# Kernel tuning notes

Hardware: AMD Instinct MI355X
Metric: run time of the kernel (lower is better)

The kernel has to match this reference:

```python
import jax, jax.numpy as jnp
import numpy as np

B, S, D, H, DFF = 4, 2048, 768, 12, 3072
DK = D // H

def setup_inputs() -> dict:
    key = jax.random.key(0)
    ks = jax.random.split(key, 16)
    sc = 0.02
    inp = {
        'src': jax.random.normal(ks[0], (B, S, D), jnp.float32),
        'mask': jnp.ones((B, 1, 1, S), jnp.int32),
        'Wq': jax.random.normal(ks[1], (D, D), jnp.float32) * sc,
        'bq': jnp.zeros((D,), jnp.float32),
        'Wk': jax.random.normal(ks[2], (D, D), jnp.float32) * sc,
        'bk': jnp.zeros((D,), jnp.float32),
        'Wv': jax.random.normal(ks[3], (D, D), jnp.float32) * sc,
        'bv': jnp.zeros((D,), jnp.float32),
        'Wo': jax.random.normal(ks[4], (D, D), jnp.float32) * sc,
        'bo': jnp.zeros((D,), jnp.float32),
        'W1': jax.random.normal(ks[5], (D, DFF), jnp.float32) * sc,
        'b1': jnp.zeros((DFF,), jnp.float32),
        'W2': jax.random.normal(ks[6], (DFF, D), jnp.float32) * sc,
        'b2': jnp.zeros((D,), jnp.float32),
        'ln1_g': jnp.ones((D,), jnp.float32), 'ln1_b': jnp.zeros((D,), jnp.float32),
        'ln2_g': jnp.ones((D,), jnp.float32), 'ln2_b': jnp.zeros((D,), jnp.float32),
    }
    return inp

def _layernorm(x, g, b, eps=1e-5):
    mu = jnp.mean(x, axis=-1, keepdims=True)
    var = jnp.mean(jnp.square(x - mu), axis=-1, keepdims=True)
    return (x - mu) * jax.lax.rsqrt(var + eps) * g + b

def reference(src, mask, Wq, bq, Wk, bk, Wv, bv, Wo, bo, W1, b1, W2, b2, ln1_g, ln1_b, ln2_g, ln2_b):
    # Multi-head self-attention (dropout in eval mode -> identity)
    q = (src @ Wq + bq).reshape(B, S, H, DK).transpose(0, 2, 1, 3)  # [B,H,S,dk]
    k = (src @ Wk + bk).reshape(B, S, H, DK).transpose(0, 2, 1, 3)
    v = (src @ Wv + bv).reshape(B, S, H, DK).transpose(0, 2, 1, 3)
    scores = jnp.einsum('bhqd,bhkd->bhqk', q, k) / jnp.sqrt(jnp.float32(DK))
    scores = jnp.where(mask == 0, jnp.float32(-1e9), scores)
    attn = jax.nn.softmax(scores, axis=-1)
    ctx = jnp.einsum('bhqk,bhkd->bhqd', attn, v)  # [B,H,S,dk]
    ctx = ctx.transpose(0, 2, 1, 3).reshape(B, S, D)
    attn_out = ctx @ Wo + bo
    x = _layernorm(src + attn_out, ln1_g, ln1_b)
    ffn = jax.nn.relu(x @ W1 + b1) @ W2 + b2
    return _layernorm(x + ffn, ln2_g, ln2_b)
```

## Files before the change

kernel.cpp:

```cpp
#include <hip/hip_runtime.h>
#include <hip/hip_bf16.h>
#include <stdint.h>

constexpr int BB = 4;
constexpr int SS = 2048;
constexpr int DD = 768;
constexpr int HH = 12;
constexpr int DKK = 64;
constexpr int DFF2 = 3072;
constexpr int MR = BB * SS;

typedef __attribute__((ext_vector_type(4))) short short4v;
typedef __attribute__((ext_vector_type(8))) short short8v;
typedef __attribute__((ext_vector_type(4))) float f32x4;
typedef __attribute__((ext_vector_type(16))) float f32x16;
typedef __attribute__((ext_vector_type(4))) float float4v;
typedef __attribute__((ext_vector_type(4))) unsigned int u32x4;

static __device__ inline short f2bs(float f) {
    __hip_bfloat16 h = __float2bfloat16(f);
    return (short)__builtin_bit_cast(unsigned short, h);
}
static __device__ inline float bs2f(short s) {
    __hip_bfloat16 h = __builtin_bit_cast(__hip_bfloat16, (unsigned short)s);
    return __bfloat162float(h);
}

static __device__ inline void glds16(const void* g, void* l) {
    __builtin_amdgcn_global_load_lds(
        (const __attribute__((address_space(1))) void*)g,
        (__attribute__((address_space(3))) void*)l, 16, 0, 0);
}

static __device__ inline unsigned cvtpk(float a, float b) {
    unsigned d;
    asm("v_cvt_pk_bf16_f32 %0, %1, %2" : "=v"(d) : "v"(a), "v"(b));
    return d;
}
static __device__ inline short8v pk4(unsigned a, unsigned b, unsigned c, unsigned d) {
    u32x4 w; w[0] = a; w[1] = b; w[2] = c; w[3] = d;
    return __builtin_bit_cast(short8v, w);
}

static __device__ inline void bar_vmcnt4() {
    __builtin_amdgcn_sched_barrier(0);
    asm volatile("s_waitcnt vmcnt(4)" ::: "memory");
    __builtin_amdgcn_s_barrier();
    __builtin_amdgcn_sched_barrier(0);
}
static __device__ inline void bar_vmcnt0() {
    __builtin_amdgcn_sched_barrier(0);
    asm volatile("s_waitcnt vmcnt(0)" ::: "memory");
    __builtin_amdgcn_s_barrier();
    __builtin_amdgcn_sched_barrier(0);
}
static __device__ inline void bar_plain() {
    __builtin_amdgcn_sched_barrier(0);
    __builtin_amdgcn_s_barrier();
    __builtin_amdgcn_sched_barrier(0);
}

__global__ __launch_bounds__(256) void cast_f32_bf16(const float* __restrict__ in,
                                                     short* __restrict__ out, int n) {
    int i = (blockIdx.x * 256 + threadIdx.x) * 4;
    if (i < n) {
        float4v v = *(const float4v*)&in[i];
        short4v o;
        o[0] = f2bs(v[0]); o[1] = f2bs(v[1]); o[2] = f2bs(v[2]); o[3] = f2bs(v[3]);
        *(short4v*)&out[i] = o;
    }
}

__global__ __launch_bounds__(256) void transpose_cast(const float* __restrict__ W,
                                                      short* __restrict__ Wt, int K, int N) {
    __shared__ float tile[32][33];
    int n0 = blockIdx.x * 32, k0 = blockIdx.y * 32;
    int tx = threadIdx.x & 31, ty = threadIdx.x >> 5;
    #pragma unroll
    for (int i = 0; i < 32; i += 8)
        tile[ty + i][tx] = W[(size_t)(k0 + ty + i) * N + n0 + tx];
    __syncthreads();
    #pragma unroll
    for (int i = 0; i < 32; i += 8)
        Wt[(size_t)(n0 + ty + i) * K + k0 + tx] = f2bs(tile[tx][ty + i]);
}

__global__ __launch_bounds__(256) void vtrans(const short* __restrict__ V,
                                              short* __restrict__ Vt) {
    __shared__ short t[64][72];
    const int tid = threadIdx.x;
    const size_t base = (size_t)blockIdx.y * SS * DKK;
    const int s0 = blockIdx.x * 64;
    int r = tid >> 3, c = (tid & 7) * 8;
    #pragma unroll
    for (int it = 0; it < 2; it++)
        *(short8v*)&t[it * 32 + r][c] =
            *(const short8v*)&V[base + (size_t)(s0 + it * 32 + r) * DKK + c];
    __syncthreads();
    int d = tid >> 2, grp = (tid & 3) * 16;
    short8v o0, o1;
    #pragma unroll
    for (int e = 0; e < 8; e++) {
        int p0 = e, p1 = 8 + e;
        o0[e] = t[grp + (p0 & 3) + 8 * ((p0 >> 2) & 1) + 4 * (p0 >> 3)][d];
        o1[e] = t[grp + (p1 & 3) + 8 * ((p1 >> 2) & 1) + 4 * (p1 >> 3)][d];
    }
    int c0 = 2 * (tid & 3), c1 = c0 + 1;
    int p0 = c0 ^ (d & 7), p1 = c1 ^ (d & 7);
    *(short8v*)&Vt[base + (size_t)d * SS + s0 + p0 * 8] = o0;
    *(short8v*)&Vt[base + (size_t)d * SS + s0 + p1 * 8] = o1;
}

template <int EPI>
__global__ __launch_bounds__(256) void gemm_bt(
    const short* __restrict__ A, const short* __restrict__ Bt,
    int Nn, int Kn,
    const float* __restrict__ bias0, const float* __restrict__ bias1,
    const float* __restrict__ bias2,
    short* __restrict__ out0, short* __restrict__ out1, short* __restrict__ out2) {
    __shared__ alignas(16) short sA[3][128 * 32];
    __shared__ alignas(16) short sB[3][128 * 32];
    const int tid = threadIdx.x;
    const int wave = tid >> 6, lane = tid & 63;
    const int g = lane >> 4, qq = lane & 15;
    const int wm = (wave >> 1) * 64, wn = (wave & 1) * 64;

    const int gx = gridDim.x;
    const int nwg = gx * gridDim.y;
    const int wgid = blockIdx.y * gx + blockIdx.x;
    const int cpx = nwg >> 3;
    const int swz = (wgid & 7) * cpx + (wgid >> 3);
    const int bx = swz % gx, by = swz / gx;
    const int m0 = by * 128, n0 = bx * 128;

    const int e0 = wave * 512 + lane * 8;
    const int r0 = e0 >> 5, c0 = e0 & 31;

    const f32x4 zero = {0.0f, 0.0f, 0.0f, 0.0f};
    f32x4 acc[4][4];
    #pragma unroll
    for (int i = 0; i < 4; i++)
        #pragma unroll
        for (int j = 0; j < 4; j++) acc[i][j] = zero;

    const int NK = Kn >> 5;
    glds16(&A[(size_t)(m0 + r0) * Kn + c0], &sA[0][wave * 512]);
    glds16(&A[(size_t)(m0 + r0 + 64) * Kn + c0], &sA[0][wave * 512 + 2048]);
    glds16(&Bt[(size_t)(n0 + r0) * Kn + c0], &sB[0][wave * 512]);
    glds16(&Bt[(size_t)(n0 + r0 + 64) * Kn + c0], &sB[0][wave * 512 + 2048]);
    __syncthreads();

    int cur = 0, nxt = 1;
    for (int kt = 0; kt < NK; ++kt) {
        if (kt + 1 < NK) {
            const int k1 = (kt + 1) * 32;
            glds16(&A[(size_t)(m0 + r0) * Kn + k1 + c0], &sA[nxt][wave * 512]);
            glds16(&A[(size_t)(m0 + r0 + 64) * Kn + k1 + c0], &sA[nxt][wave * 512 + 2048]);
            glds16(&Bt[(size_t)(n0 + r0) * Kn + k1 + c0], &sB[nxt][wave * 512]);
            glds16(&Bt[(size_t)(n0 + r0 + 64) * Kn + k1 + c0], &sB[nxt][wave * 512 + 2048]);
            bar_vmcnt4();
        } else {
            bar_vmcnt0();
        }
        short8v af[4], bf[4];
        #pragma unroll
        for (int i = 0; i < 4; i++) {
            af[i] = *(const short8v*)&sA[cur][(wm + i * 16 + qq) * 32 + 8 * g];
            bf[i] = *(const short8v*)&sB[cur][(wn + i * 16 + qq) * 32 + 8 * g];
        }
        #pragma unroll
        for (int i = 0; i < 4; i++)
            #pragma unroll
            for (int j = 0; j < 4; j++)
                acc[i][j] = __builtin_amdgcn_mfma_f32_16x16x32_bf16(af[i], bf[j], acc[i][j], 0, 0, 0);
        cur = nxt;
        nxt = (nxt == 2) ? 0 : nxt + 1;
    }

    if constexpr (EPI == 2) {
        int which = bx / 6;
        const float* bias = (which == 0) ? bias0 : ((which == 1) ? bias1 : bias2);
        short* outp = (which == 0) ? out0 : ((which == 1) ? out1 : out2);
        float scale = (which == 0) ? 0.125f * 1.44269504088896f : 1.0f;
        #pragma unroll
        for (int i = 0; i < 4; i++)
            #pragma unroll
            for (int j = 0; j < 4; j++)
                #pragma unroll
                for (int r = 0; r < 4; r++) {
                    int row = m0 + wm + i * 16 + g * 4 + r;
                    int col = n0 - which * DD + wn + j * 16 + qq;
                    float vv = (acc[i][j][r] + bias[col]) * scale;
                    int b_ = row >> 11, s_ = row & 2047;
                    int h_ = col >> 6, d_ = col & 63;
                    if (which == 1)
                        d_ = (((d_ >> 3) ^ (s_ & 7)) << 3) | (d_ & 7);
                    outp[(((size_t)(b_ * HH + h_)) * SS + s_) * DKK + d_] = f2bs(vv);
                }
    } else {
        #pragma unroll
        for (int i = 0; i < 4; i++)
            #pragma unroll
            for (int j = 0; j < 4; j++)
                #pragma unroll
                for (int r = 0; r < 4; r++) {
                    int row = m0 + wm + i * 16 + g * 4 + r;
                    int col = n0 + wn + j * 16 + qq;
                    float vv = acc[i][j][r] + bias0[col];
                    if (EPI == 1) vv = fmaxf(vv, 0.0f);
                    out0[(size_t)row * Nn + col] = f2bs(vv);
                }
    }
}

__global__ __launch_bounds__(256) void attn_kernel(
    const short* __restrict__ Q, const short* __restrict__ Kb,
    const short* __restrict__ Vt, const int* __restrict__ mask,
    short* __restrict__ ctx) {
    __shared__ alignas(16) short sK[2][64 * 64];
    __shared__ alignas(16) short sV[2][64 * 64];
    __shared__ float sAl[4][32];
    __shared__ unsigned char smask[256];
    const int tid = threadIdx.x;
    const int wave = tid >> 6, lane = tid & 63;
    const int hi = lane >> 5, ln = lane & 31;
    constexpr int NT = SS / 64;

    int flat = blockIdx.y * gridDim.x + blockIdx.x;
    int nw = (flat & 7) * 96 + (flat >> 3);
    const int bh = nw >> 4, qb = nw & 15;
    const int b_ = bh / HH, h_ = bh % HH;
    const int q0 = qb * 128 + wave * 32;
    const size_t base = (size_t)bh * SS * DKK;

    {
        const int* mp = mask + b_ * SS + tid * 8;
        unsigned char by = 0;
        #pragma unroll
        for (int e = 0; e < 8; e++) by |= (unsigned char)((mp[e] != 0) << e);
        smask[tid] = by;
    }

    short8v qf[4];
    {
        const short* qp = &Q[base + (size_t)(q0 + ln) * DKK];
        #pragma unroll
        for (int c = 0; c < 4; c++)
            qf[c] = *(const short8v*)(qp + 16 * c + 8 * hi);
    }

    f32x16 O0, O1, ZEROV;
    #pragma unroll
    for (int r = 0; r < 16; r++) { O0[r] = 0.0f; O1[r] = 0.0f; ZEROV[r] = 0.0f; }
    float lreg = 0.0f;

    const int stgrow = wave * 8 + (lane >> 3);
    const int stgc = (lane & 7) * 8;
    const int rsz = (ln & 7) << 4;

    glds16(&Kb[base + (size_t)stgrow * DKK + stgc], &sK[0][wave * 512]);
    glds16(&Kb[base + (size_t)(stgrow + 32) * DKK + stgc], &sK[0][2048 + wave * 512]);
    glds16(&Vt[base + (size_t)stgrow * SS + stgc], &sV[0][wave * 512]);
    glds16(&Vt[base + (size_t)(stgrow + 32) * SS + stgc], &sV[0][2048 + wave * 512]);
    glds16(&Kb[base + (size_t)(64 + stgrow) * DKK + stgc], &sK[1][wave * 512]);
    glds16(&Kb[base + (size_t)(64 + stgrow + 32) * DKK + stgc], &sK[1][2048 + wave * 512]);
    glds16(&Vt[base + (size_t)stgrow * SS + 64 + stgc], &sV[1][wave * 512]);
    glds16(&Vt[base + (size_t)(stgrow + 32) * SS + 64 + stgc], &sV[1][2048 + wave * 512]);
    __syncthreads();

    for (int t = 0; t < NT; ++t) {
        const int kv0 = t * 64;
        const int cur = t & 1;
        if (t) {
            if (t + 1 < NT) bar_vmcnt4();
            else bar_vmcnt0();
        }
        const char* kr0 = (const char*)&sK[cur][0] + ln * 128;
        const char* kr1 = kr0 + 32 * 128;
        const char* vr0 = (const char*)&sV[cur][0] + ln * 128;
        const char* vr1 = vr0 + 32 * 128;

        f32x16 s0, s1;
        __builtin_amdgcn_s_setprio(1);
        {
            int off = (16 * hi) ^ rsz;
            s0 = __builtin_amdgcn_mfma_f32_32x32x16_bf16(
                *(const short8v*)(kr0 + off), qf[0], ZEROV, 0, 0, 0);
            s1 = __builtin_amdgcn_mfma_f32_32x32x16_bf16(
                *(const short8v*)(kr1 + off), qf[0], ZEROV, 0, 0, 0);
        }
        #pragma unroll
        for (int c = 1; c < 4; c++) {
            int off = (32 * c + 16 * hi) ^ rsz;
            s0 = __builtin_amdgcn_mfma_f32_32x32x16_bf16(
                *(const short8v*)(kr0 + off), qf[c], s0, 0, 0, 0);
            s1 = __builtin_amdgcn_mfma_f32_32x32x16_bf16(
                *(const short8v*)(kr1 + off), qf[c], s1, 0, 0, 0);
        }
        __builtin_amdgcn_s_setprio(0);

        uint64_t mb = *(const uint64_t*)&smask[kv0 >> 3];
        if (mb != ~0ull) {
            #pragma unroll
            for (int r = 0; r < 16; r++) {
                int kvr = (r & 3) + 8 * (r >> 2) + 4 * hi;
                if (!((mb >> kvr) & 1)) s0[r] = -1.5e9f;
                if (!((mb >> (kvr + 32)) & 1)) s1[r] = -1.5e9f;
            }
        }

        float ps = 0.0f;
        unsigned w0[8], w1[8];
        #pragma unroll
        for (int r8 = 0; r8 < 8; ++r8) {
            float a0 = __builtin_amdgcn_exp2f(s0[2 * r8]);
            float a1 = __builtin_amdgcn_exp2f(s0[2 * r8 + 1]);
            ps += a0 + a1;
            w0[r8] = cvtpk(a0, a1);
            float b0 = __builtin_amdgcn_exp2f(s1[2 * r8]);
            float b1 = __builtin_amdgcn_exp2f(s1[2 * r8 + 1]);
            ps += b0 + b1;
            w1[r8] = cvtpk(b0, b1);
        }
        lreg += ps;

        short8v p00 = pk4(w0[0], w0[1], w0[2], w0[3]);
        short8v p01 = pk4(w0[4], w0[5], w0[6], w0[7]);
        short8v p10 = pk4(w1[0], w1[1], w1[2], w1[3]);
        short8v p11 = pk4(w1[4], w1[5], w1[6], w1[7]);

        __builtin_amdgcn_s_setprio(1);
        #pragma unroll
        for (int cc = 0; cc < 4; cc++) {
            int off = (32 * cc + 16 * hi) ^ rsz;
            short8v pa = (cc == 0) ? p00 : (cc == 1) ? p01 : (cc == 2) ? p10 : p11;
            O0 = __builtin_amdgcn_mfma_f32_32x32x16_bf16(
                pa, *(const short8v*)(vr0 + off), O0, 0, 0, 0);
            O1 = __builtin_amdgcn_mfma_f32_32x32x16_bf16(
                pa, *(const short8v*)(vr1 + off), O1, 0, 0, 0);
        }
        __builtin_amdgcn_s_setprio(0);

        bar_plain();
        if (t + 2 < NT) {
            const int kn = kv0 + 128;
            glds16(&Kb[base + (size_t)(kn + stgrow) * DKK + stgc], &sK[cur][wave * 512]);
            glds16(&Kb[base + (size_t)(kn + stgrow + 32) * DKK + stgc], &sK[cur][2048 + wave * 512]);
            glds16(&Vt[base + (size_t)stgrow * SS + kn + stgc], &sV[cur][wave * 512]);
            glds16(&Vt[base + (size_t)(stgrow + 32) * SS + kn + stgc], &sV[cur][2048 + wave * 512]);
        }
    }

    lreg += __shfl_xor(lreg, 32);
    sAl[wave][ln] = 1.0f / lreg;
    #pragma unroll
    for (int r = 0; r < 16; r++) {
        int rho = (r & 3) + 8 * (r >> 2) + 4 * hi;
        float li = sAl[wave][rho];
        size_t rowoff = (size_t)(b_ * SS + q0 + rho) * DD + h_ * DKK;
        ctx[rowoff + ln] = f2bs(O0[r] * li);
        ctx[rowoff + 32 + ln] = f2bs(O1[r] * li);
    }
}

template <int IN1BF, int WB, int WF>
__global__ __launch_bounds__(256) void ln_fused(
    const void* __restrict__ in1v, const short* __restrict__ in2,
    const float* __restrict__ gw, const float* __restrict__ bw,
    short* __restrict__ outb, float* __restrict__ outf) {
    const int tid = threadIdx.x;
    const int wave = tid >> 6, lane = tid & 63;
    const int row = blockIdx.x * 4 + wave;
    float4v v[3];
    #pragma unroll
    for (int i = 0; i < 3; i++) {
        int c = i * 256 + lane * 4;
        short4v b = *(const short4v*)&in2[(size_t)row * DD + c];
        if (IN1BF) {
            short4v a = *(const short4v*)&((const short*)in1v)[(size_t)row * DD + c];
            #pragma unroll
            for (int e = 0; e < 4; e++) v[i][e] = bs2f(a[e]) + bs2f(b[e]);
        } else {
            float4v a = *(const float4v*)&((const float*)in1v)[(size_t)row * DD + c];
            #pragma unroll
            for (int e = 0; e < 4; e++) v[i][e] = a[e] + bs2f(b[e]);
        }
    }
    float s = 0.0f, s2 = 0.0f;
    #pragma unroll
    for (int i = 0; i < 3; i++)
        #pragma unroll
        for (int e = 0; e < 4; e++) { s += v[i][e]; s2 += v[i][e] * v[i][e]; }
    #pragma unroll
    for (int off = 1; off < 64; off <<= 1) {
        s += __shfl_xor(s, off);
        s2 += __shfl_xor(s2, off);
    }
    float mu = s / DD;
    float var = s2 / DD - mu * mu;
    float rs = rsqrtf(var + 1e-5f);
    #pragma unroll
    for (int i = 0; i < 3; i++) {
        int c = i * 256 + lane * 4;
        float4v gv = *(const float4v*)&gw[c];
        float4v bv = *(const float4v*)&bw[c];
        float4v y;
        #pragma unroll
        for (int e = 0; e < 4; e++) y[e] = (v[i][e] - mu) * rs * gv[e] + bv[e];
        if (WB) {
            short4v o;
            #pragma unroll
            for (int e = 0; e < 4; e++) o[e] = f2bs(y[e]);
            *(short4v*)&outb[(size_t)row * DD + c] = o;
        }
        if (WF) *(float4v*)&outf[(size_t)row * DD + c] = y;
    }
}

extern "C" void kernel_launch(void* const* d_in, const int* in_sizes, int n_in,
                              void* d_out, int out_size, void* d_ws, size_t ws_size,
                              hipStream_t stream) {
    (void)in_sizes; (void)n_in; (void)out_size; (void)ws_size;
    const float* src = (const float*)d_in[0];
    const int* mask = (const int*)d_in[1];
    const float* Wq = (const float*)d_in[2];
    const float* bq = (const float*)d_in[3];
    const float* Wk = (const float*)d_in[4];
    const float* bk = (const float*)d_in[5];
    const float* Wv = (const float*)d_in[6];
    const float* bv = (const float*)d_in[7];
    const float* Wo = (const float*)d_in[8];
    const float* bo = (const float*)d_in[9];
    const float* W1 = (const float*)d_in[10];
    const float* b1 = (const float*)d_in[11];
    const float* W2 = (const float*)d_in[12];
    const float* b2 = (const float*)d_in[13];
    const float* ln1_g = (const float*)d_in[14];
    const float* ln1_b = (const float*)d_in[15];
    const float* ln2_g = (const float*)d_in[16];
    const float* ln2_b = (const float*)d_in[17];

    char* ws = (char*)d_ws;
    const size_t SB = (size_t)MR * DD * 2;
    short* src_b  = (short*)(ws);
    short* Wqkv_t = (short*)(ws + SB);
    short* qb     = (short*)(ws + SB + 3538944);
    short* kb_    = qb + (size_t)MR * DD;
    short* vb_    = kb_ + (size_t)MR * DD;
    short* ctxb   = vb_ + (size_t)MR * DD;
    short* hb     = qb;
    short* Wo_t   = (short*)(ws + SB + 3538944 + 4 * SB);
    short* x_b    = (short*)(ws + SB + 3538944 + 4 * SB + 1179648);
    short* W1_t   = (short*)((char*)x_b + SB);
    short* W2_t   = (short*)((char*)W1_t + 4718592);
    short* vt_    = x_b;
    short* attn_b = src_b;
    short* ffn_b  = src_b;

    cast_f32_bf16<<<(MR * DD) / 1024, 256, 0, stream>>>(src, src_b, MR * DD);
    transpose_cast<<<dim3(24, 24), 256, 0, stream>>>(Wq, Wqkv_t, DD, DD);
    transpose_cast<<<dim3(24, 24), 256, 0, stream>>>(Wk, Wqkv_t + DD * DD, DD, DD);
    transpose_cast<<<dim3(24, 24), 256, 0, stream>>>(Wv, Wqkv_t + 2 * DD * DD, DD, DD);
    transpose_cast<<<dim3(24, 24), 256, 0, stream>>>(Wo, Wo_t, DD, DD);
    transpose_cast<<<dim3(96, 24), 256, 0, stream>>>(W1, W1_t, DD, DFF2);
    transpose_cast<<<dim3(24, 96), 256, 0, stream>>>(W2, W2_t, DFF2, DD);

    gemm_bt<2><<<dim3(2304 / 128, MR / 128), 256, 0, stream>>>(
        src_b, Wqkv_t, 2304, DD, bq, bk, bv, qb, kb_, vb_);

    vtrans<<<dim3(SS / 64, BB * HH), 256, 0, stream>>>(vb_, vt_);

    attn_kernel<<<dim3(SS / 128, BB * HH), 256, 0, stream>>>(qb, kb_, vt_, mask, ctxb);

    gemm_bt<0><<<dim3(DD / 128, MR / 128), 256, 0, stream>>>(
        ctxb, Wo_t, DD, DD, bo, nullptr, nullptr, attn_b, nullptr, nullptr);

    ln_fused<0, 1, 0><<<MR / 4, 256, 0, stream>>>(src, attn_b, ln1_g, ln1_b, x_b, nullptr);

    gemm_bt<1><<<dim3(DFF2 / 128, MR / 128), 256, 0, stream>>>(
        x_b, W1_t, DFF2, DD, b1, nullptr, nullptr, hb, nullptr, nullptr);
    gemm_bt<0><<<dim3(DD / 128, MR / 128), 256, 0, stream>>>(
        hb, W2_t, DD, DFF2, b2, nullptr, nullptr, ffn_b, nullptr, nullptr);

    ln_fused<1, 0, 1><<<MR / 4, 256, 0, stream>>>(x_b, ffn_b, ln2_g, ln2_b, nullptr, (float*)d_out);
}
```

Measured before the change: 308.6 us.

## Triple-buffer attention K/V tiles and compute next QK scores ahead of softmax

Attention now keeps three K/V tiles in shared memory instead of two and prefetches three tiles ahead. It also software-pipelines the QK^T MFMAs, computing the next tile's scores while the current tile's softmax and PV run, so exp work can overlap matrix work. The three Q/K/V weight transpose launches are merged into one grid with a z dimension to save launch overhead. The cost is more LDS per block, which may lower occupancy, and more live registers for the extra score accumulators.

```diff
diff --git a/kernel.cpp b/kernel.cpp
--- a/kernel.cpp
+++ b/kernel.cpp
@@ -83,6 +83,23 @@
     #pragma unroll
     for (int i = 0; i < 32; i += 8)
         Wt[(size_t)(n0 + ty + i) * K + k0 + tx] = f2bs(tile[tx][ty + i]);
+}
+
+__global__ __launch_bounds__(256) void transpose_cast3(
+    const float* __restrict__ W0, const float* __restrict__ W1v,
+    const float* __restrict__ W2v, short* __restrict__ Wt) {
+    __shared__ float tile[32][33];
+    const float* W = (blockIdx.z == 0) ? W0 : (blockIdx.z == 1) ? W1v : W2v;
+    short* out = Wt + (size_t)blockIdx.z * DD * DD;
+    int n0 = blockIdx.x * 32, k0 = blockIdx.y * 32;
+    int tx = threadIdx.x & 31, ty = threadIdx.x >> 5;
+    #pragma unroll
+    for (int i = 0; i < 32; i += 8)
+        tile[ty + i][tx] = W[(size_t)(k0 + ty + i) * DD + n0 + tx];
+    __syncthreads();
+    #pragma unroll
+    for (int i = 0; i < 32; i += 8)
+        out[(size_t)(n0 + ty + i) * DD + k0 + tx] = f2bs(tile[tx][ty + i]);
 }
 
 __global__ __launch_bounds__(256) void vtrans(const short* __restrict__ V,
@@ -217,8 +234,8 @@
     const short* __restrict__ Q, const short* __restrict__ Kb,
     const short* __restrict__ Vt, const int* __restrict__ mask,
     short* __restrict__ ctx) {
-    __shared__ alignas(16) short sK[2][64 * 64];
-    __shared__ alignas(16) short sV[2][64 * 64];
+    __shared__ alignas(16) short sK[3][64 * 64];
+    __shared__ alignas(16) short sV[3][64 * 64];
     __shared__ float sAl[4][32];
     __shared__ unsigned char smask[256];
     const int tid = threadIdx.x;
@@ -258,46 +275,50 @@
     const int stgc = (lane & 7) * 8;
     const int rsz = (ln & 7) << 4;
 
-    glds16(&Kb[base + (size_t)stgrow * DKK + stgc], &sK[0][wave * 512]);
-    glds16(&Kb[base + (size_t)(stgrow + 32) * DKK + stgc], &sK[0][2048 + wave * 512]);
-    glds16(&Vt[base + (size_t)stgrow * SS + stgc], &sV[0][wave * 512]);
-    glds16(&Vt[base + (size_t)(stgrow + 32) * SS + stgc], &sV[0][2048 + wave * 512]);
-    glds16(&Kb[base + (size_t)(64 + stgrow) * DKK + stgc], &sK[1][wave * 512]);
-    glds16(&Kb[base + (size_t)(64 + stgrow + 32) * DKK + stgc], &sK[1][2048 + wave * 512]);
-    glds16(&Vt[base + (size_t)stgrow * SS + 64 + stgc], &sV[1][wave * 512]);
-    glds16(&Vt[base + (size_t)(stgrow + 32) * SS + 64 + stgc], &sV[1][2048 + wave * 512]);
+    #pragma unroll
+    for (int pt = 0; pt < 3; pt++) {
+        const int kn = pt * 64;
+        glds16(&Kb[base + (size_t)(kn + stgrow) * DKK + stgc], &sK[pt][wave * 512]);
+        glds16(&Kb[base + (size_t)(kn + stgrow + 32) * DKK + stgc], &sK[pt][2048 + wave * 512]);
+        glds16(&Vt[base + (size_t)stgrow * SS + kn + stgc], &sV[pt][wave * 512]);
+        glds16(&Vt[base + (size_t)(stgrow + 32) * SS + kn + stgc], &sV[pt][2048 + wave * 512]);
+    }
     __syncthreads();
 
+    f32x16 sn0, sn1;
+#define QK_TILE(BUF)                                                           \
+    {                                                                          \
+        const char* kq0 = (const char*)&sK[(BUF)][0] + ln * 128;               \
+        const char* kq1 = kq0 + 32 * 128;                                      \
+        __builtin_amdgcn_s_setprio(1);                                         \
+        {   int off = (16 * hi) ^ rsz;                                         \
+            sn0 = __builtin_amdgcn_mfma_f32_32x32x16_bf16(                     \
+                *(const short8v*)(kq0 + off), qf[0], ZEROV, 0, 0, 0);          \
+            sn1 = __builtin_amdgcn_mfma_f32_32x32x16_bf16(                     \
+                *(const short8v*)(kq1 + off), qf[0], ZEROV, 0, 0, 0); }        \
+        _Pragma("unroll")                                                      \
+        for (int c = 1; c < 4; c++) {                                          \
+            int off = (32 * c + 16 * hi) ^ rsz;                                \
+            sn0 = __builtin_amdgcn_mfma_f32_32x32x16_bf16(                     \
+                *(const short8v*)(kq0 + off), qf[c], sn0, 0, 0, 0);            \
+            sn1 = __builtin_amdgcn_mfma_f32_32x32x16_bf16(                     \
+                *(const short8v*)(kq1 + off), qf[c], sn1, 0, 0, 0); }          \
+        __builtin_amdgcn_s_setprio(0);                                         \
+    }
+
+    QK_TILE(0)
+
+    int bcur = 0;
     for (int t = 0; t < NT; ++t) {
         const int kv0 = t * 64;
-        const int cur = t & 1;
-        if (t) {
-            if (t + 1 < NT) bar_vmcnt4();
+        const int bn = (bcur == 2) ? 0 : bcur + 1;
+
+        f32x16 s0 = sn0, s1 = sn1;
+        if (t + 1 < NT) {
+            if (t < NT - 2) bar_vmcnt4();
             else bar_vmcnt0();
-        }
-        const char* kr0 = (const char*)&sK[cur][0] + ln * 128;
-        const char* kr1 = kr0 + 32 * 128;
-        const char* vr0 = (const char*)&sV[cur][0] + ln * 128;
-        const char* vr1 = vr0 + 32 * 128;
-
-        f32x16 s0, s1;
-        __builtin_amdgcn_s_setprio(1);
-        {
-            int off = (16 * hi) ^ rsz;
-            s0 = __builtin_amdgcn_mfma_f32_32x32x16_bf16(
-                *(const short8v*)(kr0 + off), qf[0], ZEROV, 0, 0, 0);
-            s1 = __builtin_amdgcn_mfma_f32_32x32x16_bf16(
-                *(const short8v*)(kr1 + off), qf[0], ZEROV, 0, 0, 0);
-        }
-        #pragma unroll
-        for (int c = 1; c < 4; c++) {
-            int off = (32 * c + 16 * hi) ^ rsz;
-            s0 = __builtin_amdgcn_mfma_f32_32x32x16_bf16(
-                *(const short8v*)(kr0 + off), qf[c], s0, 0, 0, 0);
-            s1 = __builtin_amdgcn_mfma_f32_32x32x16_bf16(
-                *(const short8v*)(kr1 + off), qf[c], s1, 0, 0, 0);
-        }
-        __builtin_amdgcn_s_setprio(0);
+            QK_TILE(bn)
+        }
 
         uint64_t mb = *(const uint64_t*)&smask[kv0 >> 3];
         if (mb != ~0ull) {
@@ -329,6 +350,8 @@
         short8v p10 = pk4(w1[0], w1[1], w1[2], w1[3]);
         short8v p11 = pk4(w1[4], w1[5], w1[6], w1[7]);
 
+        const char* vr0 = (const char*)&sV[bcur][0] + ln * 128;
+        const char* vr1 = vr0 + 32 * 128;
         __builtin_amdgcn_s_setprio(1);
         #pragma unroll
         for (int cc = 0; cc < 4; cc++) {
@@ -341,15 +364,17 @@
         }
         __builtin_amdgcn_s_setprio(0);
 
-        bar_plain();
-        if (t + 2 < NT) {
-            const int kn = kv0 + 128;
-            glds16(&Kb[base + (size_t)(kn + stgrow) * DKK + stgc], &sK[cur][wave * 512]);
-            glds16(&Kb[base + (size_t)(kn + stgrow + 32) * DKK + stgc], &sK[cur][2048 + wave * 512]);
-            glds16(&Vt[base + (size_t)stgrow * SS + kn + stgc], &sV[cur][wave * 512]);
-            glds16(&Vt[base + (size_t)(stgrow + 32) * SS + kn + stgc], &sV[cur][2048 + wave * 512]);
-        }
-    }
+        if (t + 3 < NT) {
+            bar_plain();
+            const int kn = kv0 + 192;
+            glds16(&Kb[base + (size_t)(kn + stgrow) * DKK + stgc], &sK[bcur][wave * 512]);
+            glds16(&Kb[base + (size_t)(kn + stgrow + 32) * DKK + stgc], &sK[bcur][2048 + wave * 512]);
+            glds16(&Vt[base + (size_t)stgrow * SS + kn + stgc], &sV[bcur][wave * 512]);
+            glds16(&Vt[base + (size_t)(stgrow + 32) * SS + kn + stgc], &sV[bcur][2048 + wave * 512]);
+        }
+        bcur = bn;
+    }
+#undef QK_TILE
 
     lreg += __shfl_xor(lreg, 32);
     sAl[wave][ln] = 1.0f / lreg;
@@ -458,9 +483,7 @@
     short* ffn_b  = src_b;
 
     cast_f32_bf16<<<(MR * DD) / 1024, 256, 0, stream>>>(src, src_b, MR * DD);
-    transpose_cast<<<dim3(24, 24), 256, 0, stream>>>(Wq, Wqkv_t, DD, DD);
-    transpose_cast<<<dim3(24, 24), 256, 0, stream>>>(Wk, Wqkv_t + DD * DD, DD, DD);
-    transpose_cast<<<dim3(24, 24), 256, 0, stream>>>(Wv, Wqkv_t + 2 * DD * DD, DD, DD);
+    transpose_cast3<<<dim3(24, 24, 3), 256, 0, stream>>>(Wq, Wk, Wv, Wqkv_t);
     transpose_cast<<<dim3(24, 24), 256, 0, stream>>>(Wo, Wo_t, DD, DD);
     transpose_cast<<<dim3(96, 24), 256, 0, stream>>>(W1, W1_t, DD, DFF2);
     transpose_cast<<<dim3(24, 96), 256, 0, stream>>>(W2, W2_t, DFF2, DD);
```

Measured after the change: 302.8 us. Within noise of the previous version (-1.9%).
